# Kernel tuning notes

Hardware: AMD Instinct MI355X
Metric: run time of the kernel (lower is better)

## Reference

```python
import jax, jax.numpy as jnp
import numpy as np

V, C, L, H, N = 32000, 1024, 2, 16, 64
B, T, FF = 2, 1024, 4096
DW, DA, DV, DG = 64, 64, 32, 128


def setup_inputs() -> dict:
    ks = iter(jax.random.split(jax.random.key(0), 64))
    def nrm(shape, s=0.02):
        return jax.random.normal(next(ks), shape, jnp.float32) * s
    def uni(shape):
        return jax.random.uniform(next(ks), shape, jnp.float32)
    return dict(
        idx=jax.random.randint(next(ks), (B, T), 0, V, dtype=jnp.int32),
        emb_w=nrm((V, C)),
        ln0_g=jnp.ones((C,), jnp.float32), ln0_b=jnp.zeros((C,), jnp.float32),
        ln1_g=jnp.ones((L, C), jnp.float32), ln1_b=jnp.zeros((L, C), jnp.float32),
        ln2_g=jnp.ones((L, C), jnp.float32), ln2_b=jnp.zeros((L, C), jnp.float32),
        lnx_g=jnp.ones((L, C), jnp.float32), lnx_b=jnp.zeros((L, C), jnp.float32),
        lnout_g=jnp.ones((C,), jnp.float32), lnout_b=jnp.zeros((C,), jnp.float32),
        x_mix=uni((L, 6, C)),
        w0=nrm((L, C), 0.3) - 0.5,
        w1=nrm((L, C, DW)), w2=nrm((L, DW, C), 0.1),
        a0=jnp.zeros((L, C), jnp.float32), a1=nrm((L, C, DA)), a2=nrm((L, DA, C), 0.1),
        v0=jnp.ones((L, C), jnp.float32), v1=nrm((L, C, DV)), v2=nrm((L, DV, C), 0.1),
        g1=nrm((L, C, DG)), g2=nrm((L, DG, C), 0.1),
        k_k=jnp.full((L, C), 0.85, jnp.float32),
        k_a=jnp.ones((L, C), jnp.float32),
        r_k=nrm((L, H, N), 0.1),
        Wr=nrm((L, C, C)), Wk=nrm((L, C, C)), Wv=nrm((L, C, C)), Wo=nrm((L, C, C)),
        ffn_xk=uni((L, C)),
        ffn_k=nrm((L, C, FF)), ffn_v=nrm((L, FF, C)),
        time_state=nrm((L, H, N, N), 0.1),
        head_w=nrm((C, V)),
    )


def _ln(x, g, b, eps=1e-5):
    m = jnp.mean(x, -1, keepdims=True)
    v = jnp.mean(jnp.square(x - m), -1, keepdims=True)
    return (x - m) * jax.lax.rsqrt(v + eps) * g + b


def _shift(x):  # time_shift: prepend zero token, drop last
    return jnp.pad(x, ((0, 0), (1, 0), (0, 0)))[:, :-1]


def _rwkv7_scan(r, k, v, w, a, b, S0):
    # r,k,v,w,a,b: (B,T,H,N); S0: (B,H,N,N) laid out [value_dim, key_dim]
    # S_t = S_{t-1} * diag(exp(w_t)) + S_{t-1} a_t b_t^T + v_t k_t^T ; y_t = S_t r_t
    def step(S, inp):
        r_, k_, v_, w_, a_, b_ = inp
        sa = jnp.einsum('bhij,bhj->bhi', S, a_)
        S = (S * jnp.exp(w_)[:, :, None, :]
             + sa[..., None] * b_[:, :, None, :]
             + v_[..., None] * k_[:, :, None, :])
        y = jnp.einsum('bhij,bhj->bhi', S, r_)
        return S, y
    xs = tuple(jnp.moveaxis(t, 1, 0) for t in (r, k, v, w, a, b))
    S, ys = jax.lax.scan(step, S0, xs)
    return jnp.moveaxis(ys, 0, 1), S  # (B,T,H,N), (B,H,N,N)


def _forward(idx, emb_w, ln0_g, ln0_b, ln1_g, ln1_b, ln2_g, ln2_b, lnx_g, lnx_b,
             lnout_g, lnout_b, x_mix, w0, w1, w2, a0, a1, a2, v0, v1, v2,
             g1, g2, k_k, k_a, r_k, Wr, Wk, Wv, Wo, ffn_xk, ffn_k, ffn_v,
             time_state, head_w):
    Bv, Tv = idx.shape
    Lh, Hh, Nh = r_k.shape
    x = emb_w[idx]                      # (B,T,C)
    v_first = jnp.zeros_like(x)
    for i in range(Lh):
        if i == 0:
            x = _ln(x, ln0_g, ln0_b)
        xin = _ln(x, ln1_g[i], ln1_b[i])
        xx = _shift(xin) - xin
        xr, xw, xk, xv, xa_, xg = (xin + xx * x_mix[i, j] for j in range(6))
        r = xr @ Wr[i]
        w = -jax.nn.softplus(-(w0[i] + jnp.tanh(xw @ w1[i]) @ w2[i])) - 0.5
        k = xk @ Wk[i]
        v = xv @ Wv[i]
        if i == 0:
            v_first = v
        else:
            v = v + (v_first - v) * jax.nn.sigmoid(v0[i] + (xv @ v1[i]) @ v2[i])
        a = jax.nn.sigmoid(a0[i] + (xa_ @ a1[i]) @ a2[i])
        g = jax.nn.sigmoid(xg @ g1[i]) @ g2[i]
        kk = (k * k_k[i]).reshape(Bv, Tv, Hh, Nh)
        kk = kk / jnp.maximum(jnp.linalg.norm(kk, axis=-1, keepdims=True), 1e-12)
        kk = kk.reshape(Bv, Tv, -1)
        k2 = k * (1.0 + (a - 1.0) * k_a[i])
        rs = lambda t: t.reshape(Bv, Tv, Hh, Nh)
        S0 = jnp.broadcast_to(time_state[i], (Bv, Hh, Nh, Nh))
        y, _S = _rwkv7_scan(rs(r), rs(k2), rs(v), rs(w), rs(-kk), rs(kk * a), S0)
        # ln_x = GroupNorm(H, C, eps=64e-5): per-head normalization
        m = y.mean(-1, keepdims=True)
        var = jnp.square(y - m).mean(-1, keepdims=True)
        y = (y - m) * jax.lax.rsqrt(var + 64e-5)
        y = y * lnx_g[i].reshape(Hh, Nh) + lnx_b[i].reshape(Hh, Nh)
        bonus = (rs(r) * rs(k2) * r_k[i]).sum(-1, keepdims=True) * rs(v)
        y = (y + bonus).reshape(Bv, Tv, -1)
        x = x + (y * g) @ Wo[i]
        # channel mix (x070 FFN)
        xc = _ln(x, ln2_g[i], ln2_b[i])
        kx = xc + (_shift(xc) - xc) * ffn_xk[i]
        x = x + jnp.square(jax.nn.relu(kx @ ffn_k[i])) @ ffn_v[i]
    return _ln(x, lnout_g, lnout_b) @ head_w


def reference(idx, emb_w, ln0_g, ln0_b, ln1_g, ln1_b, ln2_g, ln2_b, lnx_g, lnx_b,
              lnout_g, lnout_b, x_mix, w0, w1, w2, a0, a1, a2, v0, v1, v2,
              g1, g2, k_k, k_a, r_k, Wr, Wk, Wv, Wo, ffn_xk, ffn_k, ffn_v,
              time_state, head_w):
    return _forward(idx, emb_w, ln0_g, ln0_b, ln1_g, ln1_b, ln2_g, ln2_b,
                    lnx_g, lnx_b, lnout_g, lnout_b, x_mix, w0, w1, w2,
                    a0, a1, a2, v0, v1, v2, g1, g2, k_k, k_a, r_k,
                    Wr, Wk, Wv, Wo, ffn_xk, ffn_k, ffn_v, time_state, head_w)
```

## Files before the change

### kernel.cpp

```cpp
#include <hip/hip_runtime.h>
#include <hip/hip_bf16.h>
#include <math.h>

#define V_  32000
#define C_  1024
#define L_  2
#define H_  16
#define N_  64
#define B_  2
#define T_  1024
#define FF_ 4096
#define DW_ 64
#define DA_ 64
#define DV_ 32
#define DG_ 128
#define BT_  (B_*T_)
#define BTC_ (BT_*C_)

typedef float floatx4 __attribute__((ext_vector_type(4)));
typedef short shortx8 __attribute__((ext_vector_type(8)));
typedef __attribute__((address_space(1))) unsigned int gu32;
typedef __attribute__((address_space(3))) unsigned int su32;

__device__ __forceinline__ float sigf(float x){ return 1.0f/(1.0f+expf(-x)); }
__device__ __forceinline__ unsigned short f2bf(float x){
  __hip_bfloat16 h = __float2bfloat16(x);
  return *(unsigned short*)&h;
}
__device__ __forceinline__ void gload16(const void* g, void* l){
  __builtin_amdgcn_global_load_lds((const gu32*)g, (su32*)l, 16, 0, 0);
}

__device__ __forceinline__ float dpp_red16(float s){
  s += __int_as_float(__builtin_amdgcn_update_dpp(0, __float_as_int(s), 0xB1, 0xf, 0xf, true));
  s += __int_as_float(__builtin_amdgcn_update_dpp(0, __float_as_int(s), 0x4E, 0xf, 0xf, true));
  s += __int_as_float(__builtin_amdgcn_update_dpp(0, __float_as_int(s), 0x141, 0xf, 0xf, true));
  s += __int_as_float(__builtin_amdgcn_update_dpp(0, __float_as_int(s), 0x140, 0xf, 0xf, true));
  return s;
}

__global__ void k_embed(const int* __restrict__ idx, const float* __restrict__ emb,
                        float* __restrict__ x){
  int i = blockIdx.x*256 + threadIdx.x;
  if (i >= BTC_) return;
  int row = i / C_, c = i - row*C_;
  x[i] = emb[(size_t)idx[row]*C_ + c];
}

__global__ void k_ln(const float* __restrict__ x, const float* __restrict__ g,
                     const float* __restrict__ b, float* __restrict__ out){
  int row = blockIdx.x;
  const float* xr = x + (size_t)row*C_;
  float s = 0.f, s2 = 0.f;
  for (int c = threadIdx.x; c < C_; c += 256){ float v = xr[c]; s += v; s2 += v*v; }
  for (int o = 32; o > 0; o >>= 1){ s += __shfl_xor(s,o); s2 += __shfl_xor(s2,o); }
  __shared__ float w1s[4], w2s[4];
  int wid = threadIdx.x >> 6, lane = threadIdx.x & 63;
  if (lane == 0){ w1s[wid] = s; w2s[wid] = s2; }
  __syncthreads();
  if (threadIdx.x == 0){
    float a = 0.f, bb = 0.f;
    for (int i = 0; i < 4; i++){ a += w1s[i]; bb += w2s[i]; }
    w1s[0] = a; w2s[0] = bb;
  }
  __syncthreads();
  float mean = w1s[0] * (1.0f/C_);
  float var  = w2s[0] * (1.0f/C_) - mean*mean;
  float r = rsqrtf(var + 1e-5f);
  float* orow = out + (size_t)row*C_;
  for (int c = threadIdx.x; c < C_; c += 256)
    orow[c] = (xr[c]-mean)*r*g[c] + b[c];
}

__global__ void k_mix6(const float* __restrict__ xin, const float* __restrict__ mixl,
                       unsigned short* __restrict__ m6){
  int i = blockIdx.x*256 + threadIdx.x;
  if (i >= BTC_) return;
  int bt = i / C_, c = i - bt*C_;
  int t = bt % T_;
  float cur = xin[i];
  float prev = (t > 0) ? xin[i - C_] : 0.f;
  float d = prev - cur;
#pragma unroll
  for (int j = 0; j < 6; j++)
    m6[(size_t)j*BTC_ + i] = f2bf(cur + d*mixl[j*C_ + c]);
}

__global__ void k_ffnmix(const float* __restrict__ xc, const float* __restrict__ fxk,
                         unsigned short* __restrict__ kx){
  int i = blockIdx.x*256 + threadIdx.x;
  if (i >= BTC_) return;
  int bt = i / C_, c = i - bt*C_;
  int t = bt % T_;
  float cur = xc[i];
  float prev = (t > 0) ? xc[i - C_] : 0.f;
  kx[i] = f2bf(cur + (prev - cur)*fxk[c]);
}

__global__ void k_cast16(const float* __restrict__ in, unsigned short* __restrict__ out){
  int i = blockIdx.x*256 + threadIdx.x;
  if (i >= BTC_) return;
  out[i] = f2bf(in[i]);
}

__global__ void k_decay(const float* __restrict__ w0, float* __restrict__ wd){
  int i = blockIdx.x*256 + threadIdx.x;
  if (i >= BTC_) return;
  int c = i % C_;
  wd[i] = sigf(w0[c] + wd[i]) * 0.60653065971263342f;
}

__global__ void k_asig(const float* __restrict__ a0, float* __restrict__ a){
  int i = blockIdx.x*256 + threadIdx.x;
  if (i >= BTC_) return;
  int c = i % C_;
  a[i] = sigf(a0[c] + a[i]);
}

__global__ void k_vmix(const float* __restrict__ v0, const float* __restrict__ vv,
                       const float* __restrict__ vf, float* __restrict__ v){
  int i = blockIdx.x*256 + threadIdx.x;
  if (i >= BTC_) return;
  int c = i % C_;
  float s = sigf(v0[c] + vv[i]);
  v[i] = v[i] + (vf[i] - v[i])*s;
}

__global__ void k_kk(const float* __restrict__ kkw, const float* __restrict__ kaw,
                     const float* __restrict__ a, float* __restrict__ k,
                     float* __restrict__ kk, float* __restrict__ bba){
  int bth = blockIdx.x;
  int lane = threadIdx.x;
  int bt = bth / H_, h = bth - bt*H_;
  int cix = h*N_ + lane;
  size_t gi = (size_t)bt*C_ + cix;
  float kv = k[gi];
  float kkv = kv * kkw[cix];
  float ss = kkv*kkv;
  for (int o = 32; o > 0; o >>= 1) ss += __shfl_xor(ss,o);
  float nrm = fmaxf(sqrtf(ss), 1e-12f);
  float kkn = kkv / nrm;
  kk[gi] = kkn;
  float av = a[gi];
  bba[gi] = -kkn*av;
  k[gi] = kv * (1.f + (av - 1.f)*kaw[cix]);
}

#define SCHUNK 8
#define SROWS  8
__global__ __launch_bounds__(128) void k_scan(
    const float* __restrict__ r, const float* __restrict__ k2,
    const float* __restrict__ v, const float* __restrict__ wd,
    const float* __restrict__ kk, const float* __restrict__ bba,
    const float* __restrict__ S0, float* __restrict__ y){
  int bh = blockIdx.x & 31;
  int rblk = blockIdx.x >> 5;
  int b = bh / H_, h = bh - b*H_;
  int tid = threadIdx.x;
  int wave = tid >> 6, lane = tid & 63;
  int rg = tid >> 4;
  int row = rblk*SROWS + rg;
  int cg = tid & 15;
  int c0 = cg*4;

  __shared__ __attribute__((aligned(16))) float buf[2][6][SCHUNK][64];

  float S[4];
  {
    const floatx4 s0 = *(const floatx4*)&S0[((size_t)h*N_ + row)*N_ + c0];
#pragma unroll
    for (int ci = 0; ci < 4; ci++) S[ci] = s0[ci];
  }

  size_t hoff = ((size_t)b*T_)*C_ + (size_t)h*N_;

  auto do_stage = [&](int t0, int bi){
#pragma unroll
    for (int q = 0; q < 6; q++){
      int u = wave*6 + q;
      int vec = u >> 1, tt4 = (u & 1)*4;
      int tt = tt4 + (lane >> 4);
      const float* src;
      switch (vec){
        case 0: src = r;   break;
        case 1: src = k2;  break;
        case 2: src = v;   break;
        case 3: src = wd;  break;
        case 4: src = kk;  break;
        default: src = bba; break;
      }
      src += hoff + (size_t)(t0 + tt)*C_ + (size_t)((lane & 15)*4);
      gload16(src, &buf[bi][vec][tt4][0]);
    }
  };

  do_stage(0, 0);
  asm volatile("s_waitcnt vmcnt(0)" ::: "memory");
  __syncthreads();

  const int NC = T_/SCHUNK;
  for (int c = 0; c < NC; c++){
    int bi = c & 1;
    if (c + 1 < NC) do_stage((c+1)*SCHUNK, bi ^ 1);
    size_t off = hoff + (size_t)(c*SCHUNK)*C_;
#pragma unroll
    for (int tt = 0; tt < SCHUNK; tt++, off += C_){
      const floatx4 rv  = *(const floatx4*)&buf[bi][0][tt][c0];
      const floatx4 kv  = *(const floatx4*)&buf[bi][1][tt][c0];
      const float   vi  = buf[bi][2][tt][row];
      const floatx4 dd  = *(const floatx4*)&buf[bi][3][tt][c0];
      const floatx4 kkv = *(const floatx4*)&buf[bi][4][tt][c0];
      const floatx4 bav = *(const floatx4*)&buf[bi][5][tt][c0];
      float s = S[0]*kkv[0];
      s = fmaf(S[1], kkv[1], s);
      s = fmaf(S[2], kkv[2], s);
      s = fmaf(S[3], kkv[3], s);
      float sa = dpp_red16(s);
      float yy = 0.f;
#pragma unroll
      for (int ci = 0; ci < 4; ci++){
        float t0v = fmaf(vi, kv[ci], sa*bav[ci]);
        float sn = fmaf(S[ci], dd[ci], t0v);
        S[ci] = sn;
        yy = fmaf(sn, rv[ci], yy);
      }
      float yv = dpp_red16(yy);
      if (cg == 0) y[off + row] = yv;
    }
    asm volatile("s_waitcnt vmcnt(0)" ::: "memory");
    __syncthreads();
  }
}

__global__ void k_gnb(const float* __restrict__ lxg, const float* __restrict__ lxb,
                      const float* __restrict__ rk, const float* __restrict__ r,
                      const float* __restrict__ k2, const float* __restrict__ v,
                      const float* __restrict__ g, const float* __restrict__ y,
                      unsigned short* __restrict__ yg){
  int bth = blockIdx.x;
  int lane = threadIdx.x;
  int bt = bth / H_, h = bth - bt*H_;
  int cix = h*N_ + lane;
  size_t gi = (size_t)bt*C_ + cix;
  float yv = y[gi];
  float s = yv;
  for (int o = 32; o > 0; o >>= 1) s += __shfl_xor(s,o);
  float mean = s * (1.0f/N_);
  float d = yv - mean;
  float s2 = d*d;
  for (int o = 32; o > 0; o >>= 1) s2 += __shfl_xor(s2,o);
  float var = s2 * (1.0f/N_);
  float yn = d * rsqrtf(var + 64e-5f) * lxg[cix] + lxb[cix];
  float dv = r[gi]*k2[gi]*rk[h*N_ + lane];
  for (int o = 32; o > 0; o >>= 1) dv += __shfl_xor(dv,o);
  yg[gi] = f2bf((yn + dv*v[gi]) * g[gi]);
}

__global__ void k_tc(const float* __restrict__ in, unsigned short* __restrict__ out,
                     int R, int Cc, int Cpad){
  __shared__ float t[32][33];
  int c0 = blockIdx.x*32, r0 = blockIdx.y*32;
  int tx = threadIdx.x, ty = threadIdx.y;
  for (int i = ty; i < 32; i += 8){
    int r = r0+i, c = c0+tx;
    t[i][tx] = (r < R && c < Cc) ? in[(size_t)r*Cc + c] : 0.f;
  }
  __syncthreads();
  for (int i = ty; i < 32; i += 8){
    int oc = c0+i, orr = r0+tx;
    if (oc < Cpad && orr < R) out[(size_t)oc*R + orr] = f2bf(t[tx][i]);
  }
}

__global__ __launch_bounds__(256) void k_mgemm(
    const short* __restrict__ A, int lda, const short* __restrict__ Bt,
    float* __restrict__ Cf, unsigned short* __restrict__ Cb, int ldc,
    int K, int ep){
  __shared__ __attribute__((aligned(16))) short As[128*32];
  __shared__ __attribute__((aligned(16))) short Bs[128*32];
  int m0 = blockIdx.y*128, n0 = blockIdx.x*128;
  int tid = threadIdx.x, wave = tid >> 6, lane = tid & 63;
  int lhi = lane >> 4, llo = lane & 15;
  int wm = wave & 1, wn = wave >> 1;
  int arow = lane >> 2, acol = (lane & 3)*8;
  floatx4 acc[4][4];
#pragma unroll
  for (int i = 0; i < 4; i++)
#pragma unroll
    for (int j = 0; j < 4; j++) acc[i][j] = (floatx4){0.f,0.f,0.f,0.f};

  for (int k0 = 0; k0 < K; k0 += 32){
#pragma unroll
    for (int q = 0; q < 2; q++){
      int r0 = wave*32 + q*16;
      gload16(A  + (size_t)(m0 + r0 + arow)*lda + k0 + acol, As + r0*32);
      gload16(Bt + (size_t)(n0 + r0 + arow)*K   + k0 + acol, Bs + r0*32);
    }
    __syncthreads();
    shortx8 af[4], bfv[4];
#pragma unroll
    for (int mi = 0; mi < 4; mi++)
      af[mi] = *(const shortx8*)(As + ((wm*64 + mi*16 + llo)*32 + lhi*8));
#pragma unroll
    for (int nj = 0; nj < 4; nj++)
      bfv[nj] = *(const shortx8*)(Bs + ((wn*64 + nj*16 + llo)*32 + lhi*8));
#pragma unroll
    for (int mi = 0; mi < 4; mi++)
#pragma unroll
      for (int nj = 0; nj < 4; nj++)
        acc[mi][nj] = __builtin_amdgcn_mfma_f32_16x16x32_bf16(af[mi], bfv[nj], acc[mi][nj], 0, 0, 0);
    __syncthreads();
  }
#pragma unroll
  for (int mi = 0; mi < 4; mi++){
#pragma unroll
    for (int nj = 0; nj < 4; nj++){
      int gr0 = m0 + wm*64 + mi*16 + lhi*4;
      int gc  = n0 + wn*64 + nj*16 + llo;
#pragma unroll
      for (int rg = 0; rg < 4; rg++){
        size_t ci = (size_t)(gr0 + rg)*ldc + gc;
        float v = acc[mi][nj][rg];
        switch (ep){
          case 0: Cf[ci] = v; break;
          case 1: Cf[ci] += v; break;
          case 2: Cb[ci] = f2bf(v); break;
          case 3: Cb[ci] = f2bf(tanhf(v)); break;
          case 4: Cb[ci] = f2bf(sigf(v)); break;
          case 5: { float rr = fmaxf(v, 0.f); Cb[ci] = f2bf(rr*rr); } break;
        }
      }
    }
  }
}

extern "C" void kernel_launch(void* const* d_in, const int* in_sizes, int n_in,
                              void* d_out, int out_size, void* d_ws, size_t ws_size,
                              hipStream_t stream){
  const int*   idx     = (const int*)  d_in[0];
  const float* emb_w   = (const float*)d_in[1];
  const float* ln0_g   = (const float*)d_in[2];
  const float* ln0_b   = (const float*)d_in[3];
  const float* ln1_g   = (const float*)d_in[4];
  const float* ln1_b   = (const float*)d_in[5];
  const float* ln2_g   = (const float*)d_in[6];
  const float* ln2_b   = (const float*)d_in[7];
  const float* lnx_g   = (const float*)d_in[8];
  const float* lnx_b   = (const float*)d_in[9];
  const float* lnout_g = (const float*)d_in[10];
  const float* lnout_b = (const float*)d_in[11];
  const float* x_mix   = (const float*)d_in[12];
  const float* w0      = (const float*)d_in[13];
  const float* w1      = (const float*)d_in[14];
  const float* w2      = (const float*)d_in[15];
  const float* a0      = (const float*)d_in[16];
  const float* a1      = (const float*)d_in[17];
  const float* a2      = (const float*)d_in[18];
  const float* v0      = (const float*)d_in[19];
  const float* v1      = (const float*)d_in[20];
  const float* v2      = (const float*)d_in[21];
  const float* g1      = (const float*)d_in[22];
  const float* g2      = (const float*)d_in[23];
  const float* k_k     = (const float*)d_in[24];
  const float* k_a     = (const float*)d_in[25];
  const float* r_k     = (const float*)d_in[26];
  const float* Wr      = (const float*)d_in[27];
  const float* Wk      = (const float*)d_in[28];
  const float* Wv      = (const float*)d_in[29];
  const float* Wo      = (const float*)d_in[30];
  const float* ffn_xk  = (const float*)d_in[31];
  const float* ffn_k   = (const float*)d_in[32];
  const float* ffn_v   = (const float*)d_in[33];
  const float* tstate  = (const float*)d_in[34];
  const float* head_w  = (const float*)d_in[35];
  float* out = (float*)d_out;

  char* p = (char*)d_ws;
  auto alloc = [&](size_t bytes)->void*{ void* r = (void*)p; p += (bytes + 255) & ~(size_t)255; return r; };
  float* x      = (float*)alloc((size_t)BTC_*4);
  float* vfirst = (float*)alloc((size_t)BTC_*4);
  float* xin    = (float*)alloc((size_t)BTC_*4);
  float* rb     = (float*)alloc((size_t)BTC_*4);
  float* wdec   = (float*)alloc((size_t)BTC_*4);
  float* kb     = (float*)alloc((size_t)BTC_*4);
  float* vb     = (float*)alloc((size_t)BTC_*4);
  float* ab     = (float*)alloc((size_t)BTC_*4);
  float* kkb    = (float*)alloc((size_t)BTC_*4);
  float* yb     = (float*)alloc((size_t)BTC_*4);
  float* gb     = (float*)alloc((size_t)BTC_*4);
  unsigned short* act16 = (unsigned short*)alloc((size_t)6*BTC_*2);
  unsigned short* m_r = act16;
  unsigned short* m_w = act16 + 1*(size_t)BTC_;
  unsigned short* m_k = act16 + 2*(size_t)BTC_;
  unsigned short* m_v = act16 + 3*(size_t)BTC_;
  unsigned short* m_a = act16 + 4*(size_t)BTC_;
  unsigned short* m_g = act16 + 5*(size_t)BTC_;
  unsigned short* yg16  = m_r;
  unsigned short* kx16  = m_w;
  unsigned short* hid16 = m_k;
  unsigned short* xh16  = m_r;
  unsigned short* w16 = (unsigned short*)alloc((size_t)BT_*128*2);
  unsigned short* a16 = (unsigned short*)alloc((size_t)BT_*128*2);
  unsigned short* v16 = (unsigned short*)alloc((size_t)BT_*128*2);
  unsigned short* g16 = (unsigned short*)alloc((size_t)BT_*128*2);
  unsigned short *WrT[L_], *WkT[L_], *WvT[L_], *WoT[L_];
  unsigned short *w1T[L_], *a1T[L_], *v1T[L_], *g1T[L_];
  unsigned short *w2T[L_], *a2T[L_], *v2T[L_], *g2T[L_];
  unsigned short *fkT[L_], *fvT[L_];
  for (int l = 0; l < L_; l++){
    WrT[l] = (unsigned short*)alloc((size_t)C_*C_*2);
    WkT[l] = (unsigned short*)alloc((size_t)C_*C_*2);
    WvT[l] = (unsigned short*)alloc((size_t)C_*C_*2);
    WoT[l] = (unsigned short*)alloc((size_t)C_*C_*2);
    w1T[l] = (unsigned short*)alloc((size_t)128*C_*2);
    a1T[l] = (unsigned short*)alloc((size_t)128*C_*2);
    v1T[l] = (unsigned short*)alloc((size_t)128*C_*2);
    g1T[l] = (unsigned short*)alloc((size_t)128*C_*2);
    w2T[l] = (unsigned short*)alloc((size_t)C_*64*2);
    a2T[l] = (unsigned short*)alloc((size_t)C_*64*2);
    v2T[l] = (unsigned short*)alloc((size_t)C_*32*2);
    g2T[l] = (unsigned short*)alloc((size_t)C_*128*2);
    fkT[l] = (unsigned short*)alloc((size_t)FF_*C_*2);
    fvT[l] = (unsigned short*)alloc((size_t)C_*FF_*2);
  }
  unsigned short* hwT = (unsigned short*)alloc((size_t)V_*C_*2);

  dim3 blk(256);
  dim3 tcb(32, 8);
  int ewg = (BTC_ + 255)/256;

  auto MG = [&](const unsigned short* A, int lda, const unsigned short* Bt,
                float* Cf, unsigned short* Cb, int ldc, int M, int Nn, int K, int ep){
    k_mgemm<<<dim3(Nn/128, M/128), 256, 0, stream>>>(
      (const short*)A, lda, (const short*)Bt, Cf, Cb, ldc, K, ep);
  };

  for (int l = 0; l < L_; l++){
    k_tc<<<dim3(32,32), tcb, 0, stream>>>(Wr + (size_t)l*C_*C_, WrT[l], C_, C_, C_);
    k_tc<<<dim3(32,32), tcb, 0, stream>>>(Wk + (size_t)l*C_*C_, WkT[l], C_, C_, C_);
    k_tc<<<dim3(32,32), tcb, 0, stream>>>(Wv + (size_t)l*C_*C_, WvT[l], C_, C_, C_);
    k_tc<<<dim3(32,32), tcb, 0, stream>>>(Wo + (size_t)l*C_*C_, WoT[l], C_, C_, C_);
    k_tc<<<dim3(4,32),  tcb, 0, stream>>>(w1 + (size_t)l*C_*DW_, w1T[l], C_, DW_, 128);
    k_tc<<<dim3(4,32),  tcb, 0, stream>>>(a1 + (size_t)l*C_*DA_, a1T[l], C_, DA_, 128);
    k_tc<<<dim3(4,32),  tcb, 0, stream>>>(v1 + (size_t)l*C_*DV_, v1T[l], C_, DV_, 128);
    k_tc<<<dim3(4,32),  tcb, 0, stream>>>(g1 + (size_t)l*C_*DG_, g1T[l], C_, DG_, 128);
    k_tc<<<dim3(32,2),  tcb, 0, stream>>>(w2 + (size_t)l*DW_*C_, w2T[l], DW_, C_, C_);
    k_tc<<<dim3(32,2),  tcb, 0, stream>>>(a2 + (size_t)l*DA_*C_, a2T[l], DA_, C_, C_);
    k_tc<<<dim3(32,1),  tcb, 0, stream>>>(v2 + (size_t)l*DV_*C_, v2T[l], DV_, C_, C_);
    k_tc<<<dim3(32,4),  tcb, 0, stream>>>(g2 + (size_t)l*DG_*C_, g2T[l], DG_, C_, C_);
    k_tc<<<dim3(128,32),tcb, 0, stream>>>(ffn_k + (size_t)l*C_*FF_, fkT[l], C_, FF_, FF_);
    k_tc<<<dim3(32,128),tcb, 0, stream>>>(ffn_v + (size_t)l*FF_*C_, fvT[l], FF_, C_, C_);
  }
  k_tc<<<dim3(1000,32), tcb, 0, stream>>>(head_w, hwT, C_, V_, V_);

  k_embed<<<ewg, blk, 0, stream>>>(idx, emb_w, x);

  for (int l = 0; l < L_; l++){
    const float* mixl = x_mix + ((size_t)l*6)*C_;
    if (l == 0)
      k_ln<<<BT_, blk, 0, stream>>>(x, ln0_g, ln0_b, x);
    k_ln<<<BT_, blk, 0, stream>>>(x, ln1_g + l*C_, ln1_b + l*C_, xin);
    k_mix6<<<ewg, blk, 0, stream>>>(xin, mixl, act16);

    MG(m_r, C_, WrT[l], rb, 0, C_, BT_, C_, C_, 0);
    MG(m_w, C_, w1T[l], 0, w16, 128, BT_, 128, C_, 3);
    MG(m_k, C_, WkT[l], kb, 0, C_, BT_, C_, C_, 0);
    MG(m_v, C_, WvT[l], vb, 0, C_, BT_, C_, C_, 0);
    if (l > 0)
      MG(m_v, C_, v1T[l], 0, v16, 128, BT_, 128, C_, 2);
    MG(m_a, C_, a1T[l], 0, a16, 128, BT_, 128, C_, 2);
    MG(m_g, C_, g1T[l], 0, g16, 128, BT_, 128, C_, 4);

    MG(w16, 128, w2T[l], wdec, 0, C_, BT_, C_, DW_, 0);
    k_decay<<<ewg, blk, 0, stream>>>(w0 + l*C_, wdec);
    MG(a16, 128, a2T[l], ab, 0, C_, BT_, C_, DA_, 0);
    k_asig<<<ewg, blk, 0, stream>>>(a0 + l*C_, ab);
    if (l == 0){
      hipMemcpyAsync(vfirst, vb, (size_t)BTC_*4, hipMemcpyDeviceToDevice, stream);
    } else {
      MG(v16, 128, v2T[l], xin, 0, C_, BT_, C_, DV_, 0);
      k_vmix<<<ewg, blk, 0, stream>>>(v0 + l*C_, xin, vfirst, vb);
    }
    MG(g16, 128, g2T[l], gb, 0, C_, BT_, C_, DG_, 0);

    k_kk<<<BT_*H_, 64, 0, stream>>>(k_k + l*C_, k_a + l*C_, ab, kb, kkb, xin);

    k_scan<<<B_*H_*(N_/SROWS), 128, 0, stream>>>(rb, kb, vb, wdec, kkb, xin,
                                      tstate + (size_t)l*H_*N_*N_, yb);

    k_gnb<<<BT_*H_, 64, 0, stream>>>(lnx_g + l*C_, lnx_b + l*C_, r_k + (size_t)l*H_*N_,
                                     rb, kb, vb, gb, yb, yg16);

    MG(yg16, C_, WoT[l], x, 0, C_, BT_, C_, C_, 1);

    k_ln<<<BT_, blk, 0, stream>>>(x, ln2_g + l*C_, ln2_b + l*C_, xin);
    k_ffnmix<<<ewg, blk, 0, stream>>>(xin, ffn_xk + l*C_, kx16);
    MG(kx16, C_, fkT[l], 0, hid16, FF_, BT_, FF_, C_, 5);
    MG(hid16, FF_, fvT[l], x, 0, C_, BT_, C_, FF_, 1);
  }

  k_ln<<<BT_, blk, 0, stream>>>(x, lnout_g, lnout_b, xin);
  k_cast16<<<ewg, blk, 0, stream>>>(xin, xh16);
  MG(xh16, C_, hwT, out, 0, V_, BT_, V_, C_, 0);
}
```

Measured before the change: 2.384 ms.

## Fuse layernorm with token-shift mixes and GEMM epilogues; deepen scan chunk pipelining

LayerNorm is fused with the time-shift mixing kernels by recomputing the previous row's normalization in the same block. The decay, sigmoid and value-mix elementwise passes move into new GEMM epilogue modes, and the final LN writes bf16 directly, dropping the cast kernel. The scan kernel doubles its chunk size, prefetches the next timestep's LDS operands into registers, and uses partial vmcnt waits with raw barriers. Together these remove several full-tensor passes and launches, at the cost of reading each row twice in the LN kernels and extra register pressure in the scan.

```diff
diff --git a/kernel.cpp b/kernel.cpp
--- a/kernel.cpp
+++ b/kernel.cpp
@@ -48,7 +48,8 @@
 }
 
 __global__ void k_ln(const float* __restrict__ x, const float* __restrict__ g,
-                     const float* __restrict__ b, float* __restrict__ out){
+                     const float* __restrict__ b, float* __restrict__ out,
+                     unsigned short* __restrict__ out16){
   int row = blockIdx.x;
   const float* xr = x + (size_t)row*C_;
   float s = 0.f, s2 = 0.f;
@@ -67,63 +68,94 @@
   float mean = w1s[0] * (1.0f/C_);
   float var  = w2s[0] * (1.0f/C_) - mean*mean;
   float r = rsqrtf(var + 1e-5f);
-  float* orow = out + (size_t)row*C_;
-  for (int c = threadIdx.x; c < C_; c += 256)
-    orow[c] = (xr[c]-mean)*r*g[c] + b[c];
-}
-
-__global__ void k_mix6(const float* __restrict__ xin, const float* __restrict__ mixl,
-                       unsigned short* __restrict__ m6){
-  int i = blockIdx.x*256 + threadIdx.x;
-  if (i >= BTC_) return;
-  int bt = i / C_, c = i - bt*C_;
-  int t = bt % T_;
-  float cur = xin[i];
-  float prev = (t > 0) ? xin[i - C_] : 0.f;
-  float d = prev - cur;
-#pragma unroll
-  for (int j = 0; j < 6; j++)
-    m6[(size_t)j*BTC_ + i] = f2bf(cur + d*mixl[j*C_ + c]);
-}
-
-__global__ void k_ffnmix(const float* __restrict__ xc, const float* __restrict__ fxk,
-                         unsigned short* __restrict__ kx){
-  int i = blockIdx.x*256 + threadIdx.x;
-  if (i >= BTC_) return;
-  int bt = i / C_, c = i - bt*C_;
-  int t = bt % T_;
-  float cur = xc[i];
-  float prev = (t > 0) ? xc[i - C_] : 0.f;
-  kx[i] = f2bf(cur + (prev - cur)*fxk[c]);
-}
-
-__global__ void k_cast16(const float* __restrict__ in, unsigned short* __restrict__ out){
-  int i = blockIdx.x*256 + threadIdx.x;
-  if (i >= BTC_) return;
-  out[i] = f2bf(in[i]);
-}
-
-__global__ void k_decay(const float* __restrict__ w0, float* __restrict__ wd){
-  int i = blockIdx.x*256 + threadIdx.x;
-  if (i >= BTC_) return;
-  int c = i % C_;
-  wd[i] = sigf(w0[c] + wd[i]) * 0.60653065971263342f;
-}
-
-__global__ void k_asig(const float* __restrict__ a0, float* __restrict__ a){
-  int i = blockIdx.x*256 + threadIdx.x;
-  if (i >= BTC_) return;
-  int c = i % C_;
-  a[i] = sigf(a0[c] + a[i]);
-}
-
-__global__ void k_vmix(const float* __restrict__ v0, const float* __restrict__ vv,
-                       const float* __restrict__ vf, float* __restrict__ v){
-  int i = blockIdx.x*256 + threadIdx.x;
-  if (i >= BTC_) return;
-  int c = i % C_;
-  float s = sigf(v0[c] + vv[i]);
-  v[i] = v[i] + (vf[i] - v[i])*s;
+  if (out16){
+    unsigned short* orow = out16 + (size_t)row*C_;
+    for (int c = threadIdx.x; c < C_; c += 256)
+      orow[c] = f2bf((xr[c]-mean)*r*g[c] + b[c]);
+  } else {
+    float* orow = out + (size_t)row*C_;
+    for (int c = threadIdx.x; c < C_; c += 256)
+      orow[c] = (xr[c]-mean)*r*g[c] + b[c];
+  }
+}
+
+__global__ void k_lnmix(const float* __restrict__ x, const float* __restrict__ g,
+                        const float* __restrict__ b, const float* __restrict__ mixl,
+                        unsigned short* __restrict__ m6){
+  int row = blockIdx.x;
+  int t = row & (T_-1);
+  const float* xr = x + (size_t)row*C_;
+  const float* xp = xr - C_;
+  float s0=0.f,q0=0.f,s1=0.f,q1=0.f;
+  for (int c = threadIdx.x; c < C_; c += 256){
+    float v = xr[c]; s0 += v; q0 += v*v;
+    if (t > 0){ float u = xp[c]; s1 += u; q1 += u*u; }
+  }
+  for (int o=32;o>0;o>>=1){
+    s0+=__shfl_xor(s0,o); q0+=__shfl_xor(q0,o);
+    s1+=__shfl_xor(s1,o); q1+=__shfl_xor(q1,o);
+  }
+  __shared__ float rA[4], rB[4], rC[4], rD[4];
+  int wid = threadIdx.x>>6, lane = threadIdx.x&63;
+  if (lane==0){ rA[wid]=s0; rB[wid]=q0; rC[wid]=s1; rD[wid]=q1; }
+  __syncthreads();
+  if (threadIdx.x==0){
+    float a=0,bb=0,cc=0,dd=0;
+    for(int i=0;i<4;i++){a+=rA[i];bb+=rB[i];cc+=rC[i];dd+=rD[i];}
+    rA[0]=a;rB[0]=bb;rC[0]=cc;rD[0]=dd;
+  }
+  __syncthreads();
+  float m0 = rA[0]*(1.f/C_);
+  float r0 = rsqrtf(rB[0]*(1.f/C_)-m0*m0 + 1e-5f);
+  float m1=0.f, r1=0.f;
+  if (t>0){ m1 = rC[0]*(1.f/C_); r1 = rsqrtf(rD[0]*(1.f/C_)-m1*m1 + 1e-5f); }
+  size_t base = (size_t)row*C_;
+  for (int c = threadIdx.x; c < C_; c += 256){
+    float cur = (xr[c]-m0)*r0*g[c]+b[c];
+    float pv  = (t>0) ? (xp[c]-m1)*r1*g[c]+b[c] : 0.f;
+    float d = pv - cur;
+#pragma unroll
+    for (int j=0;j<6;j++)
+      m6[(size_t)j*BTC_ + base + c] = f2bf(cur + d*mixl[j*C_+c]);
+  }
+}
+
+__global__ void k_lnffn(const float* __restrict__ x, const float* __restrict__ g,
+                        const float* __restrict__ b, const float* __restrict__ fxk,
+                        unsigned short* __restrict__ kx){
+  int row = blockIdx.x;
+  int t = row & (T_-1);
+  const float* xr = x + (size_t)row*C_;
+  const float* xp = xr - C_;
+  float s0=0.f,q0=0.f,s1=0.f,q1=0.f;
+  for (int c = threadIdx.x; c < C_; c += 256){
+    float v = xr[c]; s0 += v; q0 += v*v;
+    if (t > 0){ float u = xp[c]; s1 += u; q1 += u*u; }
+  }
+  for (int o=32;o>0;o>>=1){
+    s0+=__shfl_xor(s0,o); q0+=__shfl_xor(q0,o);
+    s1+=__shfl_xor(s1,o); q1+=__shfl_xor(q1,o);
+  }
+  __shared__ float rA[4], rB[4], rC[4], rD[4];
+  int wid = threadIdx.x>>6, lane = threadIdx.x&63;
+  if (lane==0){ rA[wid]=s0; rB[wid]=q0; rC[wid]=s1; rD[wid]=q1; }
+  __syncthreads();
+  if (threadIdx.x==0){
+    float a=0,bb=0,cc=0,dd=0;
+    for(int i=0;i<4;i++){a+=rA[i];bb+=rB[i];cc+=rC[i];dd+=rD[i];}
+    rA[0]=a;rB[0]=bb;rC[0]=cc;rD[0]=dd;
+  }
+  __syncthreads();
+  float m0 = rA[0]*(1.f/C_);
+  float r0 = rsqrtf(rB[0]*(1.f/C_)-m0*m0 + 1e-5f);
+  float m1=0.f, r1=0.f;
+  if (t>0){ m1 = rC[0]*(1.f/C_); r1 = rsqrtf(rD[0]*(1.f/C_)-m1*m1 + 1e-5f); }
+  size_t base = (size_t)row*C_;
+  for (int c = threadIdx.x; c < C_; c += 256){
+    float cur = (xr[c]-m0)*r0*g[c]+b[c];
+    float pv  = (t>0) ? (xp[c]-m1)*r1*g[c]+b[c] : 0.f;
+    kx[base + c] = f2bf(cur + (pv - cur)*fxk[c]);
+  }
 }
 
 __global__ void k_kk(const float* __restrict__ kkw, const float* __restrict__ kaw,
@@ -146,7 +178,7 @@
   k[gi] = kv * (1.f + (av - 1.f)*kaw[cix]);
 }
 
-#define SCHUNK 8
+#define SCHUNK 16
 #define SROWS  8
 __global__ __launch_bounds__(128) void k_scan(
     const float* __restrict__ r, const float* __restrict__ k2,
@@ -176,9 +208,9 @@
 
   auto do_stage = [&](int t0, int bi){
 #pragma unroll
-    for (int q = 0; q < 6; q++){
-      int u = wave*6 + q;
-      int vec = u >> 1, tt4 = (u & 1)*4;
+    for (int q = 0; q < 12; q++){
+      int u = wave*12 + q;
+      int vec = u >> 2, tt4 = (u & 3)*4;
       int tt = tt4 + (lane >> 4);
       const float* src;
       switch (vec){
@@ -196,21 +228,33 @@
 
   do_stage(0, 0);
   asm volatile("s_waitcnt vmcnt(0)" ::: "memory");
-  __syncthreads();
+  __builtin_amdgcn_s_barrier();
 
   const int NC = T_/SCHUNK;
+  size_t off = hoff;
   for (int c = 0; c < NC; c++){
     int bi = c & 1;
-    if (c + 1 < NC) do_stage((c+1)*SCHUNK, bi ^ 1);
-    size_t off = hoff + (size_t)(c*SCHUNK)*C_;
+    bool more = (c + 1 < NC);
+    if (more) do_stage((c+1)*SCHUNK, bi ^ 1);
+    asm volatile("" ::: "memory");
+
+    floatx4 rv  = *(const floatx4*)&buf[bi][0][0][c0];
+    floatx4 kv  = *(const floatx4*)&buf[bi][1][0][c0];
+    float   vi  = buf[bi][2][0][row];
+    floatx4 dd  = *(const floatx4*)&buf[bi][3][0][c0];
+    floatx4 kkv = *(const floatx4*)&buf[bi][4][0][c0];
+    floatx4 bav = *(const floatx4*)&buf[bi][5][0][c0];
 #pragma unroll
     for (int tt = 0; tt < SCHUNK; tt++, off += C_){
-      const floatx4 rv  = *(const floatx4*)&buf[bi][0][tt][c0];
-      const floatx4 kv  = *(const floatx4*)&buf[bi][1][tt][c0];
-      const float   vi  = buf[bi][2][tt][row];
-      const floatx4 dd  = *(const floatx4*)&buf[bi][3][tt][c0];
-      const floatx4 kkv = *(const floatx4*)&buf[bi][4][tt][c0];
-      const floatx4 bav = *(const floatx4*)&buf[bi][5][tt][c0];
+      floatx4 rv2, kv2, dd2, kkv2, bav2; float vi2;
+      if (tt + 1 < SCHUNK){
+        rv2  = *(const floatx4*)&buf[bi][0][tt+1][c0];
+        kv2  = *(const floatx4*)&buf[bi][1][tt+1][c0];
+        vi2  = buf[bi][2][tt+1][row];
+        dd2  = *(const floatx4*)&buf[bi][3][tt+1][c0];
+        kkv2 = *(const floatx4*)&buf[bi][4][tt+1][c0];
+        bav2 = *(const floatx4*)&buf[bi][5][tt+1][c0];
+      }
       float s = S[0]*kkv[0];
       s = fmaf(S[1], kkv[1], s);
       s = fmaf(S[2], kkv[2], s);
@@ -226,9 +270,15 @@
       }
       float yv = dpp_red16(yy);
       if (cg == 0) y[off + row] = yv;
+      if (tt + 1 < SCHUNK){
+        rv = rv2; kv = kv2; vi = vi2; dd = dd2; kkv = kkv2; bav = bav2;
+      }
     }
-    asm volatile("s_waitcnt vmcnt(0)" ::: "memory");
-    __syncthreads();
+    if (more){
+      asm volatile("s_waitcnt vmcnt(16)" ::: "memory");
+      __builtin_amdgcn_sched_barrier(0);
+      __builtin_amdgcn_s_barrier();
+    }
   }
 }
 
@@ -275,7 +325,7 @@
 __global__ __launch_bounds__(256) void k_mgemm(
     const short* __restrict__ A, int lda, const short* __restrict__ Bt,
     float* __restrict__ Cf, unsigned short* __restrict__ Cb, int ldc,
-    int K, int ep){
+    int K, int ep, const float* __restrict__ ec, const float* __restrict__ e1){
   __shared__ __attribute__((aligned(16))) short As[128*32];
   __shared__ __attribute__((aligned(16))) short Bs[128*32];
   int m0 = blockIdx.y*128, n0 = blockIdx.x*128;
@@ -328,6 +378,10 @@
           case 3: Cb[ci] = f2bf(tanhf(v)); break;
           case 4: Cb[ci] = f2bf(sigf(v)); break;
           case 5: { float rr = fmaxf(v, 0.f); Cb[ci] = f2bf(rr*rr); } break;
+          case 6: Cf[ci] = sigf(ec[gc] + v) * 0.60653065971263342f; break;
+          case 7: Cf[ci] = sigf(ec[gc] + v); break;
+          case 8: { float sg = sigf(ec[gc] + v); float cv = Cf[ci];
+                    Cf[ci] = cv + (e1[ci] - cv)*sg; } break;
         }
       }
     }
@@ -427,12 +481,12 @@
 
   dim3 blk(256);
   dim3 tcb(32, 8);
-  int ewg = (BTC_ + 255)/256;
 
   auto MG = [&](const unsigned short* A, int lda, const unsigned short* Bt,
-                float* Cf, unsigned short* Cb, int ldc, int M, int Nn, int K, int ep){
+                float* Cf, unsigned short* Cb, int ldc, int M, int Nn, int K, int ep,
+                const float* ec = 0, const float* e1 = 0){
     k_mgemm<<<dim3(Nn/128, M/128), 256, 0, stream>>>(
-      (const short*)A, lda, (const short*)Bt, Cf, Cb, ldc, K, ep);
+      (const short*)A, lda, (const short*)Bt, Cf, Cb, ldc, K, ep, ec, e1);
   };
 
   for (int l = 0; l < L_; l++){
@@ -453,14 +507,14 @@
   }
   k_tc<<<dim3(1000,32), tcb, 0, stream>>>(head_w, hwT, C_, V_, V_);
 
+  int ewg = (BTC_ + 255)/256;
   k_embed<<<ewg, blk, 0, stream>>>(idx, emb_w, x);
 
   for (int l = 0; l < L_; l++){
     const float* mixl = x_mix + ((size_t)l*6)*C_;
     if (l == 0)
-      k_ln<<<BT_, blk, 0, stream>>>(x, ln0_g, ln0_b, x);
-    k_ln<<<BT_, blk, 0, stream>>>(x, ln1_g + l*C_, ln1_b + l*C_, xin);
-    k_mix6<<<ewg, blk, 0, stream>>>(xin, mixl, act16);
+      k_ln<<<BT_, blk, 0, stream>>>(x, ln0_g, ln0_b, x, (unsigned short*)0);
+    k_lnmix<<<BT_, blk, 0, stream>>>(x, ln1_g + l*C_, ln1_b + l*C_, mixl, act16);
 
     MG(m_r, C_, WrT[l], rb, 0, C_, BT_, C_, C_, 0);
     MG(m_w, C_, w1T[l], 0, w16, 128, BT_, 128, C_, 3);
@@ -471,15 +525,12 @@
     MG(m_a, C_, a1T[l], 0, a16, 128, BT_, 128, C_, 2);
     MG(m_g, C_, g1T[l], 0, g16, 128, BT_, 128, C_, 4);
 
-    MG(w16, 128, w2T[l], wdec, 0, C_, BT_, C_, DW_, 0);
-    k_decay<<<ewg, blk, 0, stream>>>(w0 + l*C_, wdec);
-    MG(a16, 128, a2T[l], ab, 0, C_, BT_, C_, DA_, 0);
-    k_asig<<<ewg, blk, 0, stream>>>(a0 + l*C_, ab);
+    MG(w16, 128, w2T[l], wdec, 0, C_, BT_, C_, DW_, 6, w0 + l*C_);
+    MG(a16, 128, a2T[l], ab,   0, C_, BT_, C_, DA_, 7, a0 + l*C_);
     if (l == 0){
       hipMemcpyAsync(vfirst, vb, (size_t)BTC_*4, hipMemcpyDeviceToDevice, stream);
     } else {
-      MG(v16, 128, v2T[l], xin, 0, C_, BT_, C_, DV_, 0);
-      k_vmix<<<ewg, blk, 0, stream>>>(v0 + l*C_, xin, vfirst, vb);
+      MG(v16, 128, v2T[l], vb, 0, C_, BT_, C_, DV_, 8, v0 + l*C_, vfirst);
     }
     MG(g16, 128, g2T[l], gb, 0, C_, BT_, C_, DG_, 0);
 
@@ -493,13 +544,11 @@
 
     MG(yg16, C_, WoT[l], x, 0, C_, BT_, C_, C_, 1);
 
-    k_ln<<<BT_, blk, 0, stream>>>(x, ln2_g + l*C_, ln2_b + l*C_, xin);
-    k_ffnmix<<<ewg, blk, 0, stream>>>(xin, ffn_xk + l*C_, kx16);
+    k_lnffn<<<BT_, blk, 0, stream>>>(x, ln2_g + l*C_, ln2_b + l*C_, ffn_xk + l*C_, kx16);
     MG(kx16, C_, fkT[l], 0, hid16, FF_, BT_, FF_, C_, 5);
     MG(hid16, FF_, fvT[l], x, 0, C_, BT_, C_, FF_, 1);
   }
 
-  k_ln<<<BT_, blk, 0, stream>>>(x, lnout_g, lnout_b, xin);
-  k_cast16<<<ewg, blk, 0, stream>>>(xin, xh16);
+  k_ln<<<BT_, blk, 0, stream>>>(x, lnout_g, lnout_b, (float*)0, xh16);
   MG(xh16, C_, hwT, out, 0, V_, BT_, V_, C_, 0);
 }
```

Result: slower. 2.640 ms (+10.7%).
